# Kernel optimization log

Hardware: AMD Instinct MI355X
Metric: run time of the kernel (lower is better)

## Reference

```python
import jax, jax.numpy as jnp
import numpy as np


def _filter_flow(img, filters, K):
    # img: [N, 2, H, W]; filters: [N, K*K, H, W] per-pixel adaptive kernels
    N, C, H, W = img.shape
    pad = (K - 1) // 2
    imgp = jnp.pad(img, ((0, 0), (0, 0), (pad, pad), (pad, pad)))
    # patches: [N, C*K*K, H, W], channel-major then row-major (dy, dx) --
    # matches torch F.unfold per single channel
    patches = jax.lax.conv_general_dilated_patches(
        imgp, (K, K), (1, 1), 'VALID',
        dimension_numbers=('NCHW', 'OIHW', 'NCHW'))
    patches = patches.reshape(N, C, K * K, H, W)
    return jnp.sum(patches * filters[:, None], axis=2)  # [N, 2, H, W]


def _grid(N, H, W, dtype):
    xx = jnp.broadcast_to(jnp.arange(W, dtype=dtype)[None, :], (H, W)) / max(W - 1, 1)
    yy = jnp.broadcast_to(jnp.arange(H, dtype=dtype)[:, None], (H, W)) / max(H - 1, 1)
    return jnp.broadcast_to(jnp.stack([xx, yy])[None], (N, 2, H, W))


def setup_inputs() -> dict:
    key = jax.random.key(0)
    k1, k2 = jax.random.split(key)
    N, K, H, W = 4, 11, 256, 256
    FF_AtoB = jax.random.uniform(k1, (N, K * K, H, W), dtype=jnp.float32)
    FF_BtoA = jax.random.uniform(k2, (N, K * K, H, W), dtype=jnp.float32)
    return {"FF_AtoB": FF_AtoB, "FF_BtoA": FF_BtoA, "filter_size": K}


def reference(FF_AtoB, FF_BtoA, filter_size):
    weight = 1.0
    N, C, H, W = FF_AtoB.shape
    K = filter_size
    grid = _grid(N, H, W, FF_AtoB.dtype)

    def cycle_loss(ff1, ff2):
        m = _filter_flow(grid, ff1, K)
        m = _filter_flow(m, ff2, K)
        diff = jnp.sqrt(jnp.sum((grid - m) ** 2, axis=1))  # [N, H, W]
        per_img = jnp.sum(diff, axis=(1, 2)) / (H * W)
        return jnp.sum(per_img) / N

    loss_ABA = cycle_loss(FF_AtoB, FF_BtoA)
    loss_BAB = cycle_loss(FF_BtoA, FF_AtoB)
    return (loss_ABA + loss_BAB) * weight
```

## Files before the change

kernel.cpp:

```cpp
#include <hip/hip_runtime.h>
#include <math.h>

#define NB    4
#define KF    11
#define KK    121
#define HH    256
#define WW    256
#define HW    (HH * WW)
#define PADK  5
#define TROWS 12
#define TW2   268
#define INVD  (1.0f / 255.0f)
#define RPB   2
#define GRID1 (NB * HH / RPB)

__global__ __launch_bounds__(256) void pass1_kernel(const float* __restrict__ F,
                                                    float* __restrict__ m1) {
    const int t   = threadIdx.x;
    const int n   = blockIdx.x / (HH / RPB);
    const int h0  = (blockIdx.x % (HH / RPB)) * RPB;
    const int sub = t >> 7;
    const int j   = t & 127;
    const int h   = h0 + sub;
    const int w0  = j * 2;

    const float2* fp = (const float2*)(F + (size_t)n * KK * HW + (size_t)h * WW + w0);

    float mk0[KF], mk1[KF];
#pragma unroll
    for (int kx = 0; kx < KF; ++kx) {
        int c0 = w0 + kx - PADK;
        mk0[kx] = (c0 >= 0 && c0 < WW) ? 1.0f : 0.0f;
        mk1[kx] = (c0 + 1 >= 0 && c0 + 1 < WW) ? 1.0f : 0.0f;
    }
    const float b0 = (float)(w0 - PADK) * INVD;

    float ax0 = 0, ay0 = 0, ax1 = 0, ay1 = 0;
    for (int ky = 0; ky < KF; ++ky) {
        int rr = h + ky - PADK;
        if (rr < 0 || rr >= HH) continue;
        float yv = (float)rr * INVD;
        const float2* fr = fp + (size_t)(ky * KF) * (HW / 2);
        float s0 = 0, s1 = 0;
#pragma unroll
        for (int kx = 0; kx < KF; ++kx) {
            float2 f = fr[(size_t)kx * (HW / 2)];
            float u0 = f.x * mk0[kx], u1 = f.y * mk1[kx];
            float xk = b0 + (float)kx * INVD;
            ax0 = fmaf(u0, xk, ax0);
            ax1 = fmaf(u1, xk + INVD, ax1);
            s0 += u0; s1 += u1;
        }
        ay0 = fmaf(yv, s0, ay0);
        ay1 = fmaf(yv, s1, ay1);
    }
    float2* ox = (float2*)(m1 + (size_t)n * 2 * HW + (size_t)h * WW + w0);
    float2* oy = (float2*)(m1 + (size_t)n * 2 * HW + HW + (size_t)h * WW + w0);
    *ox = make_float2(ax0, ax1);
    *oy = make_float2(ay0, ay1);
}

template <bool FUSE>
__global__ __launch_bounds__(256) void pass2_kernel(const float* __restrict__ F,
                                                    const float* __restrict__ m1in,
                                                    float* __restrict__ m1out,
                                                    float* __restrict__ partial) {
    __shared__ float tile[2 * TROWS * TW2];
    __shared__ float wsum[4];

    const int t   = threadIdx.x;
    const int n   = blockIdx.x / (HH / RPB);
    const int h0  = (blockIdx.x % (HH / RPB)) * RPB;
    const int sub = t >> 7;
    const int j   = t & 127;
    const int h   = h0 + sub;
    const int w0  = j * 2;

    const float* mbase = m1in + (size_t)n * 2 * HW;
    for (int i = t; i < 2 * TROWS * TW2; i += 256) {
        int ch  = i / (TROWS * TW2);
        int rem = i - ch * (TROWS * TW2);
        int r   = rem / TW2;
        int c   = rem - r * TW2;
        int rr  = h0 + r - PADK;
        int cc  = c - PADK;
        float v = 0.0f;
        if (rr >= 0 && rr < HH && cc >= 0 && cc < WW)
            v = mbase[(size_t)ch * HW + rr * WW + cc];
        tile[i] = v;
    }
    __syncthreads();

    const float2* fp = (const float2*)(F + (size_t)n * KK * HW + (size_t)h * WW + w0);

    float mk0[KF], mk1[KF];
#pragma unroll
    for (int kx = 0; kx < KF; ++kx) {
        int c0 = w0 + kx - PADK;
        mk0[kx] = (c0 >= 0 && c0 < WW) ? 1.0f : 0.0f;
        mk1[kx] = (c0 + 1 >= 0 && c0 + 1 < WW) ? 1.0f : 0.0f;
    }
    const float b0 = (float)(w0 - PADK) * INVD;

    float a1x0 = 0, a1y0 = 0, a1x1 = 0, a1y1 = 0;
    float a2x0 = 0, a2y0 = 0, a2x1 = 0, a2y1 = 0;

    for (int ky = 0; ky < KF; ++ky) {
        int rr = h + ky - PADK;
        if (rr < 0 || rr >= HH) continue;
        float yv = (float)rr * INVD;
        const float2* fr = fp + (size_t)(ky * KF) * (HW / 2);

        const float* tx = tile + (sub + ky) * TW2 + w0;
        const float* ty = tx + TROWS * TW2;
        float cx[12], cy[12];
#pragma unroll
        for (int q = 0; q < 6; ++q) {
            float2 vx = *(const float2*)(tx + 2 * q);
            float2 vy = *(const float2*)(ty + 2 * q);
            cx[2 * q] = vx.x; cx[2 * q + 1] = vx.y;
            cy[2 * q] = vy.x; cy[2 * q + 1] = vy.y;
        }

        float s0 = 0, s1 = 0;
#pragma unroll
        for (int kx = 0; kx < KF; ++kx) {
            float2 f = fr[(size_t)kx * (HW / 2)];
            if (FUSE) {
                float u0 = f.x * mk0[kx], u1 = f.y * mk1[kx];
                float xk = b0 + (float)kx * INVD;
                a1x0 = fmaf(u0, xk, a1x0);
                a1x1 = fmaf(u1, xk + INVD, a1x1);
                s0 += u0; s1 += u1;
            }
            a2x0 = fmaf(f.x, cx[kx], a2x0);
            a2x1 = fmaf(f.y, cx[kx + 1], a2x1);
            a2y0 = fmaf(f.x, cy[kx], a2y0);
            a2y1 = fmaf(f.y, cy[kx + 1], a2y1);
        }
        if (FUSE) {
            a1y0 = fmaf(yv, s0, a1y0);
            a1y1 = fmaf(yv, s1, a1y1);
        }
    }

    if (FUSE) {
        float2* ox = (float2*)(m1out + (size_t)n * 2 * HW + (size_t)h * WW + w0);
        float2* oy = (float2*)(m1out + (size_t)n * 2 * HW + HW + (size_t)h * WW + w0);
        *ox = make_float2(a1x0, a1x1);
        *oy = make_float2(a1y0, a1y1);
    }

    float gx = (float)w0 * INVD, gy = (float)h * INVD;
    float dx0 = gx - a2x0,        dy0 = gy - a2y0;
    float dx1 = gx + INVD - a2x1, dy1 = gy - a2y1;
    float d = sqrtf(dx0 * dx0 + dy0 * dy0) + sqrtf(dx1 * dx1 + dy1 * dy1);

#pragma unroll
    for (int off = 32; off > 0; off >>= 1) d += __shfl_down(d, off, 64);
    if ((t & 63) == 0) wsum[t >> 6] = d;
    __syncthreads();
    if (t == 0) partial[blockIdx.x] = wsum[0] + wsum[1] + wsum[2] + wsum[3];
}

__global__ __launch_bounds__(256) void finalize_kernel(const float* __restrict__ partial,
                                                       float* __restrict__ out) {
    __shared__ float wsum[4];
    int t = threadIdx.x;
    float s = partial[t] + partial[t + 256] + partial[t + 512] + partial[t + 768];
#pragma unroll
    for (int off = 32; off > 0; off >>= 1) s += __shfl_down(s, off, 64);
    if ((t & 63) == 0) wsum[t >> 6] = s;
    __syncthreads();
    if (t == 0)
        out[0] = (wsum[0] + wsum[1] + wsum[2] + wsum[3]) * (1.0f / ((float)HW * (float)NB));
}

extern "C" void kernel_launch(void* const* d_in, const int* in_sizes, int n_in,
                              void* d_out, int out_size, void* d_ws, size_t ws_size,
                              hipStream_t stream) {
    const float* FA = (const float*)d_in[0];
    const float* FB = (const float*)d_in[1];
    float* out = (float*)d_out;

    float* m1A = (float*)d_ws;
    float* m1B = m1A + (size_t)NB * 2 * HW;
    float* partial = m1B + (size_t)NB * 2 * HW;

    dim3 grid(GRID1), block(256);
    pass1_kernel<<<grid, block, 0, stream>>>(FA, m1A);
    pass2_kernel<true><<<grid, block, 0, stream>>>(FB, m1A, m1B, partial);
    pass2_kernel<false><<<grid, block, 0, stream>>>(FA, m1B, nullptr, partial + GRID1);

    finalize_kernel<<<1, block, 0, stream>>>(partial, out);
}
```

Baseline: 295.1 us.

## Fuse four kernels into one cooperative kernel with grid syncs and nontemporal loads

Merges pass1, both pass2 passes and the final reduction into a single cooperative launch of 512 blocks, separated by grid-wide syncs, so three kernel launch gaps disappear. The per-pixel filter loads also switch to nontemporal loads, which are meant to keep the large streamed filter arrays from displacing reused data in cache. The trade-off is that every block must be co-resident (launch bounds are set to 2 blocks per CU), and each grid sync costs time. Blocks also cannot overlap across phases the way they could between separate kernels.

```diff
diff --git a/kernel.cpp b/kernel.cpp
--- a/kernel.cpp
+++ b/kernel.cpp
@@ -1,5 +1,8 @@
 #include <hip/hip_runtime.h>
+#include <hip/hip_cooperative_groups.h>
 #include <math.h>
+
+namespace cg = cooperative_groups;
 
 #define NB    4
 #define KF    11
@@ -14,68 +17,20 @@
 #define RPB   2
 #define GRID1 (NB * HH / RPB)
 
-__global__ __launch_bounds__(256) void pass1_kernel(const float* __restrict__ F,
-                                                    float* __restrict__ m1) {
-    const int t   = threadIdx.x;
-    const int n   = blockIdx.x / (HH / RPB);
-    const int h0  = (blockIdx.x % (HH / RPB)) * RPB;
-    const int sub = t >> 7;
-    const int j   = t & 127;
-    const int h   = h0 + sub;
-    const int w0  = j * 2;
-
-    const float2* fp = (const float2*)(F + (size_t)n * KK * HW + (size_t)h * WW + w0);
-
-    float mk0[KF], mk1[KF];
-#pragma unroll
-    for (int kx = 0; kx < KF; ++kx) {
-        int c0 = w0 + kx - PADK;
-        mk0[kx] = (c0 >= 0 && c0 < WW) ? 1.0f : 0.0f;
-        mk1[kx] = (c0 + 1 >= 0 && c0 + 1 < WW) ? 1.0f : 0.0f;
-    }
-    const float b0 = (float)(w0 - PADK) * INVD;
-
-    float ax0 = 0, ay0 = 0, ax1 = 0, ay1 = 0;
-    for (int ky = 0; ky < KF; ++ky) {
-        int rr = h + ky - PADK;
-        if (rr < 0 || rr >= HH) continue;
-        float yv = (float)rr * INVD;
-        const float2* fr = fp + (size_t)(ky * KF) * (HW / 2);
-        float s0 = 0, s1 = 0;
-#pragma unroll
-        for (int kx = 0; kx < KF; ++kx) {
-            float2 f = fr[(size_t)kx * (HW / 2)];
-            float u0 = f.x * mk0[kx], u1 = f.y * mk1[kx];
-            float xk = b0 + (float)kx * INVD;
-            ax0 = fmaf(u0, xk, ax0);
-            ax1 = fmaf(u1, xk + INVD, ax1);
-            s0 += u0; s1 += u1;
-        }
-        ay0 = fmaf(yv, s0, ay0);
-        ay1 = fmaf(yv, s1, ay1);
-    }
-    float2* ox = (float2*)(m1 + (size_t)n * 2 * HW + (size_t)h * WW + w0);
-    float2* oy = (float2*)(m1 + (size_t)n * 2 * HW + HW + (size_t)h * WW + w0);
-    *ox = make_float2(ax0, ax1);
-    *oy = make_float2(ay0, ay1);
+typedef float f2v __attribute__((ext_vector_type(2)));
+
+__device__ __forceinline__ f2v ntload2(const float* p) {
+    return __builtin_nontemporal_load((const f2v*)p);
 }
 
 template <bool FUSE>
-__global__ __launch_bounds__(256) void pass2_kernel(const float* __restrict__ F,
-                                                    const float* __restrict__ m1in,
-                                                    float* __restrict__ m1out,
-                                                    float* __restrict__ partial) {
-    __shared__ float tile[2 * TROWS * TW2];
-    __shared__ float wsum[4];
-
-    const int t   = threadIdx.x;
-    const int n   = blockIdx.x / (HH / RPB);
-    const int h0  = (blockIdx.x % (HH / RPB)) * RPB;
-    const int sub = t >> 7;
-    const int j   = t & 127;
-    const int h   = h0 + sub;
-    const int w0  = j * 2;
-
+__device__ __forceinline__ void pass2_body(
+    const float* __restrict__ F, const float* __restrict__ m1in,
+    float* __restrict__ m1out, float* __restrict__ presult,
+    int n, int h0, int sub, int h, int w0, int t,
+    const float* mk0, const float* mk1, float b0,
+    float* tile, float* wsum)
+{
     const float* mbase = m1in + (size_t)n * 2 * HW;
     for (int i = t; i < 2 * TROWS * TW2; i += 256) {
         int ch  = i / (TROWS * TW2);
@@ -91,16 +46,7 @@
     }
     __syncthreads();
 
-    const float2* fp = (const float2*)(F + (size_t)n * KK * HW + (size_t)h * WW + w0);
-
-    float mk0[KF], mk1[KF];
-#pragma unroll
-    for (int kx = 0; kx < KF; ++kx) {
-        int c0 = w0 + kx - PADK;
-        mk0[kx] = (c0 >= 0 && c0 < WW) ? 1.0f : 0.0f;
-        mk1[kx] = (c0 + 1 >= 0 && c0 + 1 < WW) ? 1.0f : 0.0f;
-    }
-    const float b0 = (float)(w0 - PADK) * INVD;
+    const float* fp = F + (size_t)n * KK * HW + (size_t)h * WW + w0;
 
     float a1x0 = 0, a1y0 = 0, a1x1 = 0, a1y1 = 0;
     float a2x0 = 0, a2y0 = 0, a2x1 = 0, a2y1 = 0;
@@ -109,15 +55,15 @@
         int rr = h + ky - PADK;
         if (rr < 0 || rr >= HH) continue;
         float yv = (float)rr * INVD;
-        const float2* fr = fp + (size_t)(ky * KF) * (HW / 2);
+        const float* fr = fp + (size_t)(ky * KF) * HW;
 
         const float* tx = tile + (sub + ky) * TW2 + w0;
         const float* ty = tx + TROWS * TW2;
         float cx[12], cy[12];
 #pragma unroll
         for (int q = 0; q < 6; ++q) {
-            float2 vx = *(const float2*)(tx + 2 * q);
-            float2 vy = *(const float2*)(ty + 2 * q);
+            f2v vx = *(const f2v*)(tx + 2 * q);
+            f2v vy = *(const f2v*)(ty + 2 * q);
             cx[2 * q] = vx.x; cx[2 * q + 1] = vx.y;
             cy[2 * q] = vy.x; cy[2 * q + 1] = vy.y;
         }
@@ -125,7 +71,7 @@
         float s0 = 0, s1 = 0;
 #pragma unroll
         for (int kx = 0; kx < KF; ++kx) {
-            float2 f = fr[(size_t)kx * (HW / 2)];
+            f2v f = ntload2(fr + (size_t)kx * HW);
             if (FUSE) {
                 float u0 = f.x * mk0[kx], u1 = f.y * mk1[kx];
                 float xk = b0 + (float)kx * INVD;
@@ -145,10 +91,9 @@
     }
 
     if (FUSE) {
-        float2* ox = (float2*)(m1out + (size_t)n * 2 * HW + (size_t)h * WW + w0);
-        float2* oy = (float2*)(m1out + (size_t)n * 2 * HW + HW + (size_t)h * WW + w0);
-        *ox = make_float2(a1x0, a1x1);
-        *oy = make_float2(a1y0, a1y1);
+        f2v ox = {a1x0, a1x1}, oy = {a1y0, a1y1};
+        *(f2v*)(m1out + (size_t)n * 2 * HW + (size_t)h * WW + w0) = ox;
+        *(f2v*)(m1out + (size_t)n * 2 * HW + HW + (size_t)h * WW + w0) = oy;
     }
 
     float gx = (float)w0 * INVD, gy = (float)h * INVD;
@@ -160,20 +105,87 @@
     for (int off = 32; off > 0; off >>= 1) d += __shfl_down(d, off, 64);
     if ((t & 63) == 0) wsum[t >> 6] = d;
     __syncthreads();
-    if (t == 0) partial[blockIdx.x] = wsum[0] + wsum[1] + wsum[2] + wsum[3];
-}
-
-__global__ __launch_bounds__(256) void finalize_kernel(const float* __restrict__ partial,
-                                                       float* __restrict__ out) {
+    if (t == 0) *presult = wsum[0] + wsum[1] + wsum[2] + wsum[3];
+}
+
+__global__ __launch_bounds__(256, 2) void fused_kernel(
+    const float* __restrict__ FA, const float* __restrict__ FB,
+    float* __restrict__ m1A, float* __restrict__ m1B,
+    float* __restrict__ partial, float* __restrict__ out)
+{
+    __shared__ float tile[2 * TROWS * TW2];
     __shared__ float wsum[4];
-    int t = threadIdx.x;
-    float s = partial[t] + partial[t + 256] + partial[t + 512] + partial[t + 768];
-#pragma unroll
-    for (int off = 32; off > 0; off >>= 1) s += __shfl_down(s, off, 64);
-    if ((t & 63) == 0) wsum[t >> 6] = s;
-    __syncthreads();
-    if (t == 0)
-        out[0] = (wsum[0] + wsum[1] + wsum[2] + wsum[3]) * (1.0f / ((float)HW * (float)NB));
+    cg::grid_group grid = cg::this_grid();
+
+    const int t   = threadIdx.x;
+    const int bid = blockIdx.x;
+    const int n   = bid / (HH / RPB);
+    const int h0  = (bid % (HH / RPB)) * RPB;
+    const int sub = t >> 7;
+    const int j   = t & 127;
+    const int h   = h0 + sub;
+    const int w0  = j * 2;
+
+    float mk0[KF], mk1[KF];
+#pragma unroll
+    for (int kx = 0; kx < KF; ++kx) {
+        int c0 = w0 + kx - PADK;
+        mk0[kx] = (c0 >= 0 && c0 < WW) ? 1.0f : 0.0f;
+        mk1[kx] = (c0 + 1 >= 0 && c0 + 1 < WW) ? 1.0f : 0.0f;
+    }
+    const float b0 = (float)(w0 - PADK) * INVD;
+
+    {
+        const float* fp = FA + (size_t)n * KK * HW + (size_t)h * WW + w0;
+        float ax0 = 0, ay0 = 0, ax1 = 0, ay1 = 0;
+        for (int ky = 0; ky < KF; ++ky) {
+            int rr = h + ky - PADK;
+            if (rr < 0 || rr >= HH) continue;
+            float yv = (float)rr * INVD;
+            const float* fr = fp + (size_t)(ky * KF) * HW;
+            float s0 = 0, s1 = 0;
+#pragma unroll
+            for (int kx = 0; kx < KF; ++kx) {
+                f2v f = ntload2(fr + (size_t)kx * HW);
+                float u0 = f.x * mk0[kx], u1 = f.y * mk1[kx];
+                float xk = b0 + (float)kx * INVD;
+                ax0 = fmaf(u0, xk, ax0);
+                ax1 = fmaf(u1, xk + INVD, ax1);
+                s0 += u0; s1 += u1;
+            }
+            ay0 = fmaf(yv, s0, ay0);
+            ay1 = fmaf(yv, s1, ay1);
+        }
+        f2v vx = {ax0, ax1}, vy = {ay0, ay1};
+        *(f2v*)(m1A + (size_t)n * 2 * HW + (size_t)h * WW + w0) = vx;
+        *(f2v*)(m1A + (size_t)n * 2 * HW + HW + (size_t)h * WW + w0) = vy;
+    }
+
+    __threadfence();
+    grid.sync();
+
+    pass2_body<true>(FB, m1A, m1B, partial + bid,
+                     n, h0, sub, h, w0, t, mk0, mk1, b0, tile, wsum);
+
+    __threadfence();
+    grid.sync();
+
+    pass2_body<false>(FA, m1B, nullptr, partial + GRID1 + bid,
+                      n, h0, sub, h, w0, t, mk0, mk1, b0, tile, wsum);
+
+    __threadfence();
+    grid.sync();
+
+    if (bid == 0) {
+        float s = partial[t] + partial[t + 256] + partial[t + 512] + partial[t + 768];
+#pragma unroll
+        for (int off = 32; off > 0; off >>= 1) s += __shfl_down(s, off, 64);
+        if ((t & 63) == 0) wsum[t >> 6] = s;
+        __syncthreads();
+        if (t == 0)
+            out[0] = (wsum[0] + wsum[1] + wsum[2] + wsum[3]) *
+                     (1.0f / ((float)HW * (float)NB));
+    }
 }
 
 extern "C" void kernel_launch(void* const* d_in, const int* in_sizes, int n_in,
@@ -187,10 +199,8 @@
     float* m1B = m1A + (size_t)NB * 2 * HW;
     float* partial = m1B + (size_t)NB * 2 * HW;
 
-    dim3 grid(GRID1), block(256);
-    pass1_kernel<<<grid, block, 0, stream>>>(FA, m1A);
-    pass2_kernel<true><<<grid, block, 0, stream>>>(FB, m1A, m1B, partial);
-    pass2_kernel<false><<<grid, block, 0, stream>>>(FA, m1B, nullptr, partial + GRID1);
-
-    finalize_kernel<<<1, block, 0, stream>>>(partial, out);
-}
+    void* args[] = {(void*)&FA, (void*)&FB, (void*)&m1A, (void*)&m1B,
+                    (void*)&partial, (void*)&out};
+    hipLaunchCooperativeKernel((void*)fused_kernel, dim3(GRID1), dim3(256),
+                               args, 0, stream);
+}
```

New measurement: 607.5 us. 2.06x slower.

## Merge both cycle directions into two wide kernels and batch filter loads

Applied to the files above, without the earlier changes.

Replaces the three-kernel chain, in which the middle kernel fused the first pass of one cycle with the second pass of the other, with two kernels that each process both cycle directions over a doubled grid. Filter taps for a row are loaded into registers before use to raise memory-level parallelism. The intent is a wider grid and one fewer launch. The cost is that the fused reuse of one filter tensor is lost, so total filter reads rise from three tensors to four.

```diff
diff --git a/kernel.cpp b/kernel.cpp
--- a/kernel.cpp
+++ b/kernel.cpp
@@ -7,24 +7,31 @@
 #define HH    256
 #define WW    256
 #define HW    (HH * WW)
+#define HW2   (HW / 2)
 #define PADK  5
-#define TROWS 12
+#define RPB   2
+#define TROWS (RPB + KF - 1)
 #define TW2   268
 #define INVD  (1.0f / 255.0f)
-#define RPB   2
-#define GRID1 (NB * HH / RPB)
+#define HALF  (NB * HH / RPB)
 
-__global__ __launch_bounds__(256) void pass1_kernel(const float* __restrict__ F,
-                                                    float* __restrict__ m1) {
+__global__ __launch_bounds__(256) void passX_kernel(const float* __restrict__ FA,
+                                                    const float* __restrict__ FB,
+                                                    float* __restrict__ m1A,
+                                                    float* __restrict__ m1B) {
+    const int bid = blockIdx.x;
+    const bool dirA = (bid < HALF);
+    const int b = dirA ? bid : bid - HALF;
+    const float* F  = dirA ? FA : FB;
+    float*       m1 = dirA ? m1A : m1B;
+
     const int t   = threadIdx.x;
-    const int n   = blockIdx.x / (HH / RPB);
-    const int h0  = (blockIdx.x % (HH / RPB)) * RPB;
+    const int n   = b / (HH / RPB);
+    const int h0  = (b % (HH / RPB)) * RPB;
     const int sub = t >> 7;
     const int j   = t & 127;
     const int h   = h0 + sub;
     const int w0  = j * 2;
-
-    const float2* fp = (const float2*)(F + (size_t)n * KK * HW + (size_t)h * WW + w0);
 
     float mk0[KF], mk1[KF];
 #pragma unroll
@@ -35,18 +42,25 @@
     }
     const float b0 = (float)(w0 - PADK) * INVD;
 
-    float ax0 = 0, ay0 = 0, ax1 = 0, ay1 = 0;
+    const float2* fp = (const float2*)(F + (size_t)n * KK * HW + (size_t)h * WW + w0);
+
+    float ax0 = 0, ax1 = 0, ay0 = 0, ay1 = 0;
     for (int ky = 0; ky < KF; ++ky) {
         int rr = h + ky - PADK;
         if (rr < 0 || rr >= HH) continue;
         float yv = (float)rr * INVD;
-        const float2* fr = fp + (size_t)(ky * KF) * (HW / 2);
+        const float2* fr = fp + (size_t)(ky * KF) * HW2;
+
+        float2 fq[KF];
+#pragma unroll
+        for (int kx = 0; kx < KF; ++kx) fq[kx] = fr[(size_t)kx * HW2];
+
         float s0 = 0, s1 = 0;
 #pragma unroll
         for (int kx = 0; kx < KF; ++kx) {
-            float2 f = fr[(size_t)kx * (HW / 2)];
+            float2 f = fq[kx];
+            float xk = b0 + (float)kx * INVD;
             float u0 = f.x * mk0[kx], u1 = f.y * mk1[kx];
-            float xk = b0 + (float)kx * INVD;
             ax0 = fmaf(u0, xk, ax0);
             ax1 = fmaf(u1, xk + INVD, ax1);
             s0 += u0; s1 += u1;
@@ -54,23 +68,27 @@
         ay0 = fmaf(yv, s0, ay0);
         ay1 = fmaf(yv, s1, ay1);
     }
-    float2* ox = (float2*)(m1 + (size_t)n * 2 * HW + (size_t)h * WW + w0);
-    float2* oy = (float2*)(m1 + (size_t)n * 2 * HW + HW + (size_t)h * WW + w0);
-    *ox = make_float2(ax0, ax1);
-    *oy = make_float2(ay0, ay1);
+    *(float2*)(m1 + (size_t)n * 2 * HW + (size_t)h * WW + w0)      = make_float2(ax0, ax1);
+    *(float2*)(m1 + (size_t)n * 2 * HW + HW + (size_t)h * WW + w0) = make_float2(ay0, ay1);
 }
 
-template <bool FUSE>
-__global__ __launch_bounds__(256) void pass2_kernel(const float* __restrict__ F,
-                                                    const float* __restrict__ m1in,
-                                                    float* __restrict__ m1out,
+__global__ __launch_bounds__(256) void passY_kernel(const float* __restrict__ FA,
+                                                    const float* __restrict__ FB,
+                                                    const float* __restrict__ m1A,
+                                                    const float* __restrict__ m1B,
                                                     float* __restrict__ partial) {
-    __shared__ float tile[2 * TROWS * TW2];
+    __shared__ __align__(16) float tile[2 * TROWS * TW2];
     __shared__ float wsum[4];
 
+    const int bid = blockIdx.x;
+    const bool dirA = (bid < HALF);
+    const int b = dirA ? bid : bid - HALF;
+    const float* F    = dirA ? FB : FA;
+    const float* m1in = dirA ? m1A : m1B;
+
     const int t   = threadIdx.x;
-    const int n   = blockIdx.x / (HH / RPB);
-    const int h0  = (blockIdx.x % (HH / RPB)) * RPB;
+    const int n   = b / (HH / RPB);
+    const int h0  = (b % (HH / RPB)) * RPB;
     const int sub = t >> 7;
     const int j   = t & 127;
     const int h   = h0 + sub;
@@ -93,23 +111,15 @@
 
     const float2* fp = (const float2*)(F + (size_t)n * KK * HW + (size_t)h * WW + w0);
 
-    float mk0[KF], mk1[KF];
-#pragma unroll
-    for (int kx = 0; kx < KF; ++kx) {
-        int c0 = w0 + kx - PADK;
-        mk0[kx] = (c0 >= 0 && c0 < WW) ? 1.0f : 0.0f;
-        mk1[kx] = (c0 + 1 >= 0 && c0 + 1 < WW) ? 1.0f : 0.0f;
-    }
-    const float b0 = (float)(w0 - PADK) * INVD;
-
-    float a1x0 = 0, a1y0 = 0, a1x1 = 0, a1y1 = 0;
-    float a2x0 = 0, a2y0 = 0, a2x1 = 0, a2y1 = 0;
-
+    float a2x0 = 0, a2x1 = 0, a2y0 = 0, a2y1 = 0;
     for (int ky = 0; ky < KF; ++ky) {
         int rr = h + ky - PADK;
         if (rr < 0 || rr >= HH) continue;
-        float yv = (float)rr * INVD;
-        const float2* fr = fp + (size_t)(ky * KF) * (HW / 2);
+        const float2* fr = fp + (size_t)(ky * KF) * HW2;
+
+        float2 fq[KF];
+#pragma unroll
+        for (int kx = 0; kx < KF; ++kx) fq[kx] = fr[(size_t)kx * HW2];
 
         const float* tx = tile + (sub + ky) * TW2 + w0;
         const float* ty = tx + TROWS * TW2;
@@ -122,33 +132,14 @@
             cy[2 * q] = vy.x; cy[2 * q + 1] = vy.y;
         }
 
-        float s0 = 0, s1 = 0;
 #pragma unroll
         for (int kx = 0; kx < KF; ++kx) {
-            float2 f = fr[(size_t)kx * (HW / 2)];
-            if (FUSE) {
-                float u0 = f.x * mk0[kx], u1 = f.y * mk1[kx];
-                float xk = b0 + (float)kx * INVD;
-                a1x0 = fmaf(u0, xk, a1x0);
-                a1x1 = fmaf(u1, xk + INVD, a1x1);
-                s0 += u0; s1 += u1;
-            }
+            float2 f = fq[kx];
             a2x0 = fmaf(f.x, cx[kx], a2x0);
             a2x1 = fmaf(f.y, cx[kx + 1], a2x1);
             a2y0 = fmaf(f.x, cy[kx], a2y0);
             a2y1 = fmaf(f.y, cy[kx + 1], a2y1);
         }
-        if (FUSE) {
-            a1y0 = fmaf(yv, s0, a1y0);
-            a1y1 = fmaf(yv, s1, a1y1);
-        }
-    }
-
-    if (FUSE) {
-        float2* ox = (float2*)(m1out + (size_t)n * 2 * HW + (size_t)h * WW + w0);
-        float2* oy = (float2*)(m1out + (size_t)n * 2 * HW + HW + (size_t)h * WW + w0);
-        *ox = make_float2(a1x0, a1x1);
-        *oy = make_float2(a1y0, a1y1);
     }
 
     float gx = (float)w0 * INVD, gy = (float)h * INVD;
@@ -160,7 +151,7 @@
     for (int off = 32; off > 0; off >>= 1) d += __shfl_down(d, off, 64);
     if ((t & 63) == 0) wsum[t >> 6] = d;
     __syncthreads();
-    if (t == 0) partial[blockIdx.x] = wsum[0] + wsum[1] + wsum[2] + wsum[3];
+    if (t == 0) partial[bid] = wsum[0] + wsum[1] + wsum[2] + wsum[3];
 }
 
 __global__ __launch_bounds__(256) void finalize_kernel(const float* __restrict__ partial,
@@ -187,10 +178,7 @@
     float* m1B = m1A + (size_t)NB * 2 * HW;
     float* partial = m1B + (size_t)NB * 2 * HW;
 
-    dim3 grid(GRID1), block(256);
-    pass1_kernel<<<grid, block, 0, stream>>>(FA, m1A);
-    pass2_kernel<true><<<grid, block, 0, stream>>>(FB, m1A, m1B, partial);
-    pass2_kernel<false><<<grid, block, 0, stream>>>(FA, m1B, nullptr, partial + GRID1);
-
-    finalize_kernel<<<1, block, 0, stream>>>(partial, out);
+    passX_kernel<<<dim3(2 * HALF), dim3(256), 0, stream>>>(FA, FB, m1A, m1B);
+    passY_kernel<<<dim3(2 * HALF), dim3(256), 0, stream>>>(FA, FB, m1A, m1B, partial);
+    finalize_kernel<<<1, dim3(256), 0, stream>>>(partial, out);
 }
```

Measured after the change: 307.0 us. 1.04x slower.
